# Optimization experiments

Hardware: AMD Instinct MI355X
Metric: run time of the kernel (lower is better)

Reference implementation:

```python
import jax, jax.numpy as jnp
import numpy as np

NEG_SLOPE = 0.2

def gat_conv(x, src, dst, W, a_src, a_dst, b, heads, out_ch, num_nodes):
    # Linear projection per head: [N, H, C]
    h = (x @ W).reshape(num_nodes, heads, out_ch)
    # Per-node attention logits: [N, H]
    s_src = jnp.sum(h * a_src[None, :, :], axis=-1)
    s_dst = jnp.sum(h * a_dst[None, :, :], axis=-1)
    # Per-edge attention score, LeakyReLU(0.2): [E, H]
    e = jax.nn.leaky_relu(s_src[src] + s_dst[dst], negative_slope=NEG_SLOPE)
    # Segment softmax over incoming edges of each destination node
    e_max = jax.ops.segment_max(e, dst, num_segments=num_nodes)
    e_exp = jnp.exp(e - e_max[dst])
    denom = jax.ops.segment_sum(e_exp, dst, num_segments=num_nodes)
    alpha = e_exp / (denom[dst] + 1e-16)  # [E, H]
    # Weighted message aggregation: [N, H, C]
    msg = h[src] * alpha[:, :, None]
    out = jax.ops.segment_sum(msg, dst, num_segments=num_nodes)
    # Concat heads + bias
    return out.reshape(num_nodes, heads * out_ch) + b


def setup_inputs() -> dict:
    key = jax.random.key(0)
    ks = jax.random.split(key, 9)
    N, E = 50000, 1000000
    x = jax.random.normal(ks[0], (N, 300), dtype=jnp.float32)
    edge_index = jax.random.randint(ks[1], (2, E), 0, N, dtype=jnp.int64)
    W1 = jax.random.normal(ks[2], (300, 64), dtype=jnp.float32) * 0.05
    a_src1 = jax.random.normal(ks[3], (8, 8), dtype=jnp.float32) * 0.1
    a_dst1 = jax.random.normal(ks[4], (8, 8), dtype=jnp.float32) * 0.1
    b1 = jnp.zeros((64,), dtype=jnp.float32)
    W2 = jax.random.normal(ks[5], (64, 64), dtype=jnp.float32) * 0.1
    a_src2 = jax.random.normal(ks[6], (1, 64), dtype=jnp.float32) * 0.1
    a_dst2 = jax.random.normal(ks[7], (1, 64), dtype=jnp.float32) * 0.1
    b2 = jnp.zeros((64,), dtype=jnp.float32)
    return {"x": x, "edge_index": edge_index, "W1": W1, "a_src1": a_src1,
            "a_dst1": a_dst1, "b1": b1, "W2": W2, "a_src2": a_src2,
            "a_dst2": a_dst2, "b2": b2}


def reference(x, edge_index, W1, a_src1, a_dst1, b1, W2, a_src2, a_dst2, b2):
    N = x.shape[0]
    src, dst = edge_index[0], edge_index[1]
    # eval mode: dropouts are identity
    h = gat_conv(x, src, dst, W1, a_src1, a_dst1, b1, heads=8, out_ch=8, num_nodes=N)
    h = jax.nn.elu(h)
    out = gat_conv(h, src, dst, W2, a_src2, a_dst2, b2, heads=1, out_ch=64, num_nodes=N)
    return out
```

## Files before the change

### kernel.cpp

```cpp
#include <hip/hip_runtime.h>
#include <math.h>

#define NN 50000
#define NE 1000000
#define NCB 977
#define NGB 782
#define TOTB (NCB + NGB)

typedef __bf16 bf16x8 __attribute__((ext_vector_type(8)));
typedef float f32x4 __attribute__((ext_vector_type(4)));

__device__ inline unsigned short f2bf(float f) {
    unsigned u = __float_as_uint(f);
    u += 0x7FFFu + ((u >> 16) & 1u);
    return (unsigned short)(u >> 16);
}
__device__ inline float bf2f(unsigned short s) {
    return __uint_as_float(((unsigned)s) << 16);
}
__device__ inline float bflo(unsigned r) { return __uint_as_float(r << 16); }
__device__ inline float bfhi(unsigned r) { return __uint_as_float(r & 0xffff0000u); }

__global__ __launch_bounds__(256) void prep_init(const float* __restrict__ W1,
        const float* __restrict__ W2, unsigned short* __restrict__ Bt1,
        unsigned short* __restrict__ Bt2, int* __restrict__ cnt)
{
    int bid = blockIdx.x;
    if (bid < 96) {
        int t = bid * 256 + threadIdx.x;
        if (t < 64 * 320) {
            int c = t / 320, k = t % 320;
            Bt1[t] = (k < 300) ? f2bf(W1[k * 64 + c]) : (unsigned short)0;
        } else {
            int i = t - 64 * 320;
            int c = i >> 6, k = i & 63;
            Bt2[i] = f2bf(W2[k * 64 + c]);
        }
    } else {
        int idx = (bid - 96) * 256 + threadIdx.x;
        int4 z = {0, 0, 0, 0};
        for (int i = idx; i < NN * 4; i += 64 * 256)
            ((int4*)cnt)[i] = z;
    }
}

__global__ __launch_bounds__(256) void k1_count_gemm(
        const int* __restrict__ ei, int* __restrict__ cnt,
        unsigned char* __restrict__ pos,
        const float* __restrict__ A, const unsigned short* __restrict__ Bt,
        unsigned short* __restrict__ hb,
        const float* __restrict__ asrc, const float* __restrict__ adst,
        float* __restrict__ ss, float* __restrict__ sd)
{
    __shared__ unsigned short lds[5120];
    const int tid = threadIdx.x;
    const int bid = blockIdx.x;
    int cidx, gidx;
    if (bid < 2 * NGB) {
        if (bid & 1) { gidx = bid >> 1; cidx = -1; }
        else         { cidx = bid >> 1; gidx = -1; }
    } else { cidx = NGB + (bid - 2 * NGB); gidx = -1; }

    if (cidx >= 0) {
        int e = (cidx * 256 + tid) * 4;
        if (e >= NE) return;
        int4 d = *(const int4*)(ei + NE + e);
        int p0 = atomicAdd(&cnt[d.x << 4], 1);
        int p1 = atomicAdd(&cnt[d.y << 4], 1);
        int p2 = atomicAdd(&cnt[d.z << 4], 1);
        int p3 = atomicAdd(&cnt[d.w << 4], 1);
        uchar4 pk;
        pk.x = (unsigned char)p0; pk.y = (unsigned char)p1;
        pk.z = (unsigned char)p2; pk.w = (unsigned char)p3;
        *(uchar4*)(pos + e) = pk;
        return;
    }

    const int row0 = gidx * 64;
    const int lane = tid & 63, w = tid >> 6;
    const int quad = lane >> 4, mm = lane & 15;
    const int sr = tid >> 2, q8 = (tid & 3) * 8;
    const int gsr = row0 + sr;
    const int K = 300, KT = 10, Kpad = 320, M = NN;

    f32x4 acc[4];
    #pragma unroll
    for (int i = 0; i < 4; ++i) acc[i] = (f32x4){0.f, 0.f, 0.f, 0.f};

    for (int kt = 0; kt < KT; ++kt) {
        const int k0 = kt * 32;
        int4 apack = {0, 0, 0, 0};
        if (gsr < M) {
            const float* ap = A + (size_t)gsr * K + k0 + q8;
            unsigned short* up = (unsigned short*)&apack;
            if (k0 + q8 + 7 < K) {
                float4 v0 = *(const float4*)ap;
                float4 v1 = *(const float4*)(ap + 4);
                up[0]=f2bf(v0.x); up[1]=f2bf(v0.y); up[2]=f2bf(v0.z); up[3]=f2bf(v0.w);
                up[4]=f2bf(v1.x); up[5]=f2bf(v1.y); up[6]=f2bf(v1.z); up[7]=f2bf(v1.w);
            } else {
                #pragma unroll
                for (int j = 0; j < 8; ++j)
                    up[j] = (k0 + q8 + j < K) ? f2bf(ap[j]) : (unsigned short)0;
            }
        }
        *(int4*)(lds + sr * 40 + q8) = apack;
        *(int4*)(lds + 2560 + sr * 40 + q8) =
            *(const int4*)(Bt + (size_t)sr * Kpad + k0 + q8);
        __syncthreads();
        bf16x8 af = *(const bf16x8*)(lds + (w * 16 + mm) * 40 + quad * 8);
        #pragma unroll
        for (int nt = 0; nt < 4; ++nt) {
            bf16x8 bfv = *(const bf16x8*)(lds + 2560 + (nt * 16 + mm) * 40 + quad * 8);
            acc[nt] = __builtin_amdgcn_mfma_f32_16x16x32_bf16(af, bfv, acc[nt], 0, 0, 0);
        }
        __syncthreads();
    }
    #pragma unroll
    for (int nt = 0; nt < 4; ++nt)
        #pragma unroll
        for (int reg = 0; reg < 4; ++reg)
            lds[w * 1152 + (quad * 4 + reg) * 72 + nt * 16 + mm] = f2bf(acc[nt][reg]);
    __syncthreads();
    const int cg = (tid & 3) * 16;
    const unsigned short* crow = lds + (sr >> 4) * 1152 + (sr & 15) * 72;
    if (gsr < M) {
        *(int4*)(hb + (size_t)gsr * 64 + cg)     = *(const int4*)(crow + cg);
        *(int4*)(hb + (size_t)gsr * 64 + cg + 8) = *(const int4*)(crow + cg + 8);
    }
    #pragma unroll
    for (int hh = 0; hh < 2; ++hh) {
        int hd = (tid & 3) + hh * 4;
        float pss = 0.f, psd = 0.f;
        #pragma unroll
        for (int c = 0; c < 8; ++c) {
            float hv = bf2f(crow[hd * 8 + c]);
            pss += hv * asrc[hd * 8 + c];
            psd += hv * adst[hd * 8 + c];
        }
        if (gsr < M) { ss[gsr * 8 + hd] = pss; sd[gsr * 8 + hd] = psd; }
    }
}

__global__ __launch_bounds__(256) void gemm_l2(const unsigned short* __restrict__ A,
        const unsigned short* __restrict__ Bt, unsigned short* __restrict__ hb,
        const float* __restrict__ asrc, const float* __restrict__ adst,
        float* __restrict__ ss, float* __restrict__ sd)
{
    __shared__ unsigned short lds[5120];
    const int tid  = threadIdx.x;
    const int row0 = blockIdx.x * 64;
    const int lane = tid & 63, w = tid >> 6;
    const int quad = lane >> 4, mm = lane & 15;
    const int sr = tid >> 2, q8 = (tid & 3) * 8;
    const int gsr = row0 + sr;
    const int K = 64, KT = 2, Kpad = 64, M = NN;

    f32x4 acc[4];
    #pragma unroll
    for (int i = 0; i < 4; ++i) acc[i] = (f32x4){0.f, 0.f, 0.f, 0.f};

    for (int kt = 0; kt < KT; ++kt) {
        const int k0 = kt * 32;
        int4 apack = {0, 0, 0, 0};
        if (gsr < M) apack = *(const int4*)(A + (size_t)gsr * K + k0 + q8);
        *(int4*)(lds + sr * 40 + q8) = apack;
        *(int4*)(lds + 2560 + sr * 40 + q8) =
            *(const int4*)(Bt + (size_t)sr * Kpad + k0 + q8);
        __syncthreads();
        bf16x8 af = *(const bf16x8*)(lds + (w * 16 + mm) * 40 + quad * 8);
        #pragma unroll
        for (int nt = 0; nt < 4; ++nt) {
            bf16x8 bfv = *(const bf16x8*)(lds + 2560 + (nt * 16 + mm) * 40 + quad * 8);
            acc[nt] = __builtin_amdgcn_mfma_f32_16x16x32_bf16(af, bfv, acc[nt], 0, 0, 0);
        }
        __syncthreads();
    }
    #pragma unroll
    for (int nt = 0; nt < 4; ++nt)
        #pragma unroll
        for (int reg = 0; reg < 4; ++reg)
            lds[w * 1152 + (quad * 4 + reg) * 72 + nt * 16 + mm] = f2bf(acc[nt][reg]);
    __syncthreads();
    const int cg = (tid & 3) * 16;
    const unsigned short* crow = lds + (sr >> 4) * 1152 + (sr & 15) * 72;
    if (gsr < M) {
        *(int4*)(hb + (size_t)gsr * 64 + cg)     = *(const int4*)(crow + cg);
        *(int4*)(hb + (size_t)gsr * 64 + cg + 8) = *(const int4*)(crow + cg + 8);
    }
    int p = tid & 3;
    float pss = 0.f, psd = 0.f;
    #pragma unroll
    for (int c = 0; c < 16; ++c) {
        float hv = bf2f(crow[p * 16 + c]);
        pss += hv * asrc[p * 16 + c];
        psd += hv * adst[p * 16 + c];
    }
    pss += __shfl_xor(pss, 1); psd += __shfl_xor(psd, 1);
    pss += __shfl_xor(pss, 2); psd += __shfl_xor(psd, 2);
    if (p == 0 && gsr < M) { ss[gsr] = pss; sd[gsr] = psd; }
}

__global__ __launch_bounds__(1024) void scan1(const int* __restrict__ cnt,
        int* __restrict__ excl, int* __restrict__ sums)
{
    __shared__ int buf[1024];
    int tid = threadIdx.x;
    int i = blockIdx.x * 1024 + tid;
    int v = (i < NN) ? cnt[i << 4] : 0;
    buf[tid] = v;
    __syncthreads();
    #pragma unroll
    for (int off = 1; off < 1024; off <<= 1) {
        int t = (tid >= off) ? buf[tid - off] : 0;
        __syncthreads();
        buf[tid] += t;
        __syncthreads();
    }
    if (i < NN) excl[i] = buf[tid] - v;
    if (tid == 1023) sums[blockIdx.x] = buf[1023];
}

__global__ __launch_bounds__(1024) void scan23(const int* __restrict__ excl,
        const int* __restrict__ sums, int* __restrict__ rowptr)
{
    int off = 0;
    for (int j = 0; j < (int)blockIdx.x; ++j) off += sums[j];
    int i = blockIdx.x * 1024 + threadIdx.x;
    if (i < NN) rowptr[i] = excl[i] + off;
    if (i == 0) rowptr[NN] = NE;
}

__global__ __launch_bounds__(256) void scatter_k(const int* __restrict__ ei,
        const int* __restrict__ rowptr, const unsigned char* __restrict__ pos,
        unsigned short* __restrict__ col)
{
    int e = (blockIdx.x * 256 + threadIdx.x) * 4;
    if (e >= NE) return;
    int4 s = *(const int4*)(ei + e);
    int4 d = *(const int4*)(ei + NE + e);
    uchar4 p = *(const uchar4*)(pos + e);
    int r0 = rowptr[d.x], r1 = rowptr[d.y], r2 = rowptr[d.z], r3 = rowptr[d.w];
    col[r0 + p.x] = (unsigned short)s.x;
    col[r1 + p.y] = (unsigned short)s.y;
    col[r2 + p.z] = (unsigned short)s.z;
    col[r3 + p.w] = (unsigned short)s.w;
}

#define LEAKY(s) ((s) > 0.f ? (s) : 0.2f * (s))

__global__ __launch_bounds__(256) void agg_l1(const int* __restrict__ rowptr,
        const unsigned short* __restrict__ col, const unsigned short* __restrict__ hb,
        const float* __restrict__ ss, const float* __restrict__ sd,
        const float* __restrict__ b, unsigned short* __restrict__ out)
{
    int n = (blockIdx.x * 256 + threadIdx.x) >> 6;
    int lane = threadIdx.x & 63;
    if (n >= NN) return;
    const int es = lane >> 4;
    const int cg = (lane & 15) << 2;
    const int hd = cg >> 3;
    float sdst = sd[n * 8 + hd];
    int r0 = rowptr[n], r1 = rowptr[n + 1];
    f32x4 acc = {0.f, 0.f, 0.f, 0.f};
    float dsum = 0.f;
    for (int i = r0; i < r1; i += 16) {
        int av[4]; bool vv[4];
        #pragma unroll
        for (int u = 0; u < 4; ++u) {
            int e = i + u * 4 + es;
            vv[u] = e < r1;
            av[u] = (int)col[vv[u] ? e : r0];
        }
        uint2 rr[4]; float sv[4];
        #pragma unroll
        for (int u = 0; u < 4; ++u) {
            rr[u] = *(const uint2*)(hb + av[u] * 64 + cg);
            sv[u] = ss[av[u] * 8 + hd];
        }
        #pragma unroll
        for (int u = 0; u < 4; ++u) {
            float wv = vv[u] ? __expf(LEAKY(sv[u] + sdst)) : 0.f;
            acc[0] += wv * bflo(rr[u].x);
            acc[1] += wv * bfhi(rr[u].x);
            acc[2] += wv * bflo(rr[u].y);
            acc[3] += wv * bfhi(rr[u].y);
            dsum += wv;
        }
    }
    #pragma unroll
    for (int m = 16; m <= 32; m <<= 1) {
        acc[0] += __shfl_xor(acc[0], m); acc[1] += __shfl_xor(acc[1], m);
        acc[2] += __shfl_xor(acc[2], m); acc[3] += __shfl_xor(acc[3], m);
        dsum += __shfl_xor(dsum, m);
    }
    if (es == 0) {
        float inv = 1.f / (dsum + 1e-16f);
        float v0 = acc[0] * inv + b[cg + 0]; v0 = v0 > 0.f ? v0 : __expf(v0) - 1.f;
        float v1 = acc[1] * inv + b[cg + 1]; v1 = v1 > 0.f ? v1 : __expf(v1) - 1.f;
        float v2 = acc[2] * inv + b[cg + 2]; v2 = v2 > 0.f ? v2 : __expf(v2) - 1.f;
        float v3 = acc[3] * inv + b[cg + 3]; v3 = v3 > 0.f ? v3 : __expf(v3) - 1.f;
        unsigned o01 = (unsigned)f2bf(v0) | ((unsigned)f2bf(v1) << 16);
        unsigned o23 = (unsigned)f2bf(v2) | ((unsigned)f2bf(v3) << 16);
        *(uint2*)(out + n * 64 + cg) = make_uint2(o01, o23);
    }
}

__global__ __launch_bounds__(256) void agg_l2(const int* __restrict__ rowptr,
        const unsigned short* __restrict__ col, const unsigned short* __restrict__ hb,
        const float* __restrict__ ss, const float* __restrict__ sd,
        const float* __restrict__ b, float* __restrict__ out)
{
    int n = (blockIdx.x * 256 + threadIdx.x) >> 6;
    int lane = threadIdx.x & 63;
    if (n >= NN) return;
    const int es = lane >> 4;
    const int cg = (lane & 15) << 2;
    float sdst = sd[n];
    int r0 = rowptr[n], r1 = rowptr[n + 1];
    f32x4 acc = {0.f, 0.f, 0.f, 0.f};
    float dsum = 0.f;
    for (int i = r0; i < r1; i += 16) {
        int av[4]; bool vv[4];
        #pragma unroll
        for (int u = 0; u < 4; ++u) {
            int e = i + u * 4 + es;
            vv[u] = e < r1;
            av[u] = (int)col[vv[u] ? e : r0];
        }
        uint2 rr[4]; float sv[4];
        #pragma unroll
        for (int u = 0; u < 4; ++u) {
            rr[u] = *(const uint2*)(hb + av[u] * 64 + cg);
            sv[u] = ss[av[u]];
        }
        #pragma unroll
        for (int u = 0; u < 4; ++u) {
            float wv = vv[u] ? __expf(LEAKY(sv[u] + sdst)) : 0.f;
            acc[0] += wv * bflo(rr[u].x);
            acc[1] += wv * bfhi(rr[u].x);
            acc[2] += wv * bflo(rr[u].y);
            acc[3] += wv * bfhi(rr[u].y);
            dsum += wv;
        }
    }
    #pragma unroll
    for (int m = 16; m <= 32; m <<= 1) {
        acc[0] += __shfl_xor(acc[0], m); acc[1] += __shfl_xor(acc[1], m);
        acc[2] += __shfl_xor(acc[2], m); acc[3] += __shfl_xor(acc[3], m);
        dsum += __shfl_xor(dsum, m);
    }
    if (es == 0) {
        float inv = 1.f / (dsum + 1e-16f);
        float4 o;
        o.x = acc[0] * inv + b[cg + 0];
        o.y = acc[1] * inv + b[cg + 1];
        o.z = acc[2] * inv + b[cg + 2];
        o.w = acc[3] * inv + b[cg + 3];
        *(float4*)(out + n * 64 + cg) = o;
    }
}

extern "C" void kernel_launch(void* const* d_in, const int* in_sizes, int n_in,
                              void* d_out, int out_size, void* d_ws, size_t ws_size,
                              hipStream_t stream)
{
    const float* x      = (const float*)d_in[0];
    const int*   ei     = (const int*)d_in[1];
    const float* W1     = (const float*)d_in[2];
    const float* a_src1 = (const float*)d_in[3];
    const float* a_dst1 = (const float*)d_in[4];
    const float* b1     = (const float*)d_in[5];
    const float* W2     = (const float*)d_in[6];
    const float* a_src2 = (const float*)d_in[7];
    const float* a_dst2 = (const float*)d_in[8];
    const float* b2     = (const float*)d_in[9];
    float* out = (float*)d_out;

    char* wp = (char*)d_ws;
    unsigned short* hb  = (unsigned short*)wp;  wp += (size_t)NN * 64 * 2;
    unsigned short* P1b = (unsigned short*)wp;  wp += (size_t)NN * 64 * 2;
    unsigned short* Bt1 = (unsigned short*)wp;  wp += (size_t)64 * 320 * 2;
    unsigned short* Bt2 = (unsigned short*)wp;  wp += (size_t)64 * 64 * 2;
    float* ss1 = (float*)wp;  wp += (size_t)NN * 8 * 4;
    float* sd1 = (float*)wp;  wp += (size_t)NN * 8 * 4;
    int* cnt    = (int*)wp;  wp += (size_t)NN * 64;
    int* excl   = (int*)wp;  wp += (size_t)NN * 4;
    int* sums   = (int*)wp;  wp += 64 * 4;
    int* rowptr = (int*)wp;  wp += (size_t)(NN + 4) * 4;
    unsigned short* col = (unsigned short*)wp;  wp += (size_t)(NE + 8) * 2;
    unsigned char*  pos = (unsigned char*)wp;   wp += (size_t)NE;
    float* ss2 = ss1;
    float* sd2 = ss1 + NN;

    const int NB = (NN + 1023) / 1024;

    prep_init<<<160, 256, 0, stream>>>(W1, W2, Bt1, Bt2, cnt);
    k1_count_gemm<<<TOTB, 256, 0, stream>>>(
        ei, cnt, pos, x, Bt1, hb, a_src1, a_dst1, ss1, sd1);
    scan1<<<NB, 1024, 0, stream>>>(cnt, excl, sums);
    scan23<<<NB, 1024, 0, stream>>>(excl, sums, rowptr);
    scatter_k<<<(NE / 4 + 255) / 256, 256, 0, stream>>>(ei, rowptr, pos, col);

    agg_l1<<<(NN * 64 + 255) / 256, 256, 0, stream>>>(rowptr, col, hb, ss1, sd1, b1, P1b);
    gemm_l2<<<(NN + 63) / 64, 256, 0, stream>>>(P1b, Bt2, hb, a_src2, a_dst2, ss2, sd2);
    agg_l2<<<(NN * 64 + 255) / 256, 256, 0, stream>>>(rowptr, col, hb, ss2, sd2, b2, out);
}
```

Baseline: 246.3 us.

## Replace global atomic degree counting with LDS-privatized per-chunk histograms

Edge destination counting now runs in 128 blocks, each owning one edge chunk and one node range, and counts with shared-memory atomics instead of global atomics on padded counters. Per-chunk counts go to global memory, and scan1 builds per-node prefix offsets across chunks, which scatter adds when placing CSR columns. This removes global atomic contention and the counter-zeroing pass. In exchange, every counting block reads its whole edge chunk while keeping only 1/8 of it, and a 3.2MB prefix array is added that scatter must gather from.

```diff
diff --git a/kernel.cpp b/kernel.cpp
--- a/kernel.cpp
+++ b/kernel.cpp
@@ -3,9 +3,14 @@
 
 #define NN 50000
 #define NE 1000000
-#define NCB 977
+#define EC 16
+#define CSH 16
+#define WR 8
+#define RNG 6250
+#define RPAD 6272
+#define NCNT (EC * WR)
 #define NGB 782
-#define TOTB (NCB + NGB)
+#define TOTB (NCNT + NGB)
 
 typedef __bf16 bf16x8 __attribute__((ext_vector_type(8)));
 typedef float f32x4 __attribute__((ext_vector_type(4)));
@@ -23,24 +28,16 @@
 
 __global__ __launch_bounds__(256) void prep_init(const float* __restrict__ W1,
         const float* __restrict__ W2, unsigned short* __restrict__ Bt1,
-        unsigned short* __restrict__ Bt2, int* __restrict__ cnt)
-{
-    int bid = blockIdx.x;
-    if (bid < 96) {
-        int t = bid * 256 + threadIdx.x;
-        if (t < 64 * 320) {
-            int c = t / 320, k = t % 320;
-            Bt1[t] = (k < 300) ? f2bf(W1[k * 64 + c]) : (unsigned short)0;
-        } else {
-            int i = t - 64 * 320;
-            int c = i >> 6, k = i & 63;
-            Bt2[i] = f2bf(W2[k * 64 + c]);
-        }
+        unsigned short* __restrict__ Bt2)
+{
+    int t = blockIdx.x * 256 + threadIdx.x;
+    if (t < 64 * 320) {
+        int c = t / 320, k = t % 320;
+        Bt1[t] = (k < 300) ? f2bf(W1[k * 64 + c]) : (unsigned short)0;
     } else {
-        int idx = (bid - 96) * 256 + threadIdx.x;
-        int4 z = {0, 0, 0, 0};
-        for (int i = idx; i < NN * 4; i += 64 * 256)
-            ((int4*)cnt)[i] = z;
+        int i = t - 64 * 320;
+        int c = i >> 6, k = i & 63;
+        Bt2[i] = f2bf(W2[k * 64 + c]);
     }
 }
 
@@ -52,31 +49,36 @@
         const float* __restrict__ asrc, const float* __restrict__ adst,
         float* __restrict__ ss, float* __restrict__ sd)
 {
-    __shared__ unsigned short lds[5120];
+    __shared__ __align__(16) int sm[RNG];
     const int tid = threadIdx.x;
     const int bid = blockIdx.x;
-    int cidx, gidx;
-    if (bid < 2 * NGB) {
-        if (bid & 1) { gidx = bid >> 1; cidx = -1; }
-        else         { cidx = bid >> 1; gidx = -1; }
-    } else { cidx = NGB + (bid - 2 * NGB); gidx = -1; }
-
-    if (cidx >= 0) {
-        int e = (cidx * 256 + tid) * 4;
-        if (e >= NE) return;
-        int4 d = *(const int4*)(ei + NE + e);
-        int p0 = atomicAdd(&cnt[d.x << 4], 1);
-        int p1 = atomicAdd(&cnt[d.y << 4], 1);
-        int p2 = atomicAdd(&cnt[d.z << 4], 1);
-        int p3 = atomicAdd(&cnt[d.w << 4], 1);
-        uchar4 pk;
-        pk.x = (unsigned char)p0; pk.y = (unsigned char)p1;
-        pk.z = (unsigned char)p2; pk.w = (unsigned char)p3;
-        *(uchar4*)(pos + e) = pk;
+
+    if (bid < NCNT) {
+        const int c = bid >> 3, w = bid & 7;
+        const int lo = w * RNG;
+        for (int j = tid; j < RNG; j += 256) sm[j] = 0;
+        __syncthreads();
+        const int base = c << CSH;
+        for (int it = 0; it < (1 << CSH) / 1024; ++it) {
+            int e = base + (it * 256 + tid) * 4;
+            if (e < NE) {
+                int4 d = *(const int4*)(ei + NE + e);
+                unsigned t0 = (unsigned)(d.x - lo), t1 = (unsigned)(d.y - lo);
+                unsigned t2 = (unsigned)(d.z - lo), t3 = (unsigned)(d.w - lo);
+                if (t0 < RNG) pos[e]     = (unsigned char)atomicAdd(&sm[t0], 1);
+                if (t1 < RNG) pos[e + 1] = (unsigned char)atomicAdd(&sm[t1], 1);
+                if (t2 < RNG) pos[e + 2] = (unsigned char)atomicAdd(&sm[t2], 1);
+                if (t3 < RNG) pos[e + 3] = (unsigned char)atomicAdd(&sm[t3], 1);
+            }
+        }
+        __syncthreads();
+        int* dstp = cnt + (size_t)bid * RPAD;
+        for (int j = tid; j < RNG; j += 256) dstp[j] = sm[j];
         return;
     }
 
-    const int row0 = gidx * 64;
+    unsigned short* lds = (unsigned short*)sm;
+    const int row0 = (bid - NCNT) * 64;
     const int lane = tid & 63, w = tid >> 6;
     const int quad = lane >> 4, mm = lane & 15;
     const int sr = tid >> 2, q8 = (tid & 3) * 8;
@@ -202,12 +204,28 @@
 }
 
 __global__ __launch_bounds__(1024) void scan1(const int* __restrict__ cnt,
-        int* __restrict__ excl, int* __restrict__ sums)
+        int* __restrict__ excl, int* __restrict__ sums, int* __restrict__ rpre)
 {
     __shared__ int buf[1024];
     int tid = threadIdx.x;
     int i = blockIdx.x * 1024 + tid;
-    int v = (i < NN) ? cnt[i << 4] : 0;
+    int v = 0;
+    if (i < NN) {
+        int w = i / RNG;
+        int j = i - w * RNG;
+        int run = 0;
+        int pre[EC];
+        #pragma unroll
+        for (int c = 0; c < EC; ++c) {
+            pre[c] = run;
+            run += cnt[(size_t)(c * 8 + w) * RPAD + j];
+        }
+        v = run;
+        #pragma unroll
+        for (int q = 0; q < EC / 4; ++q)
+            *(int4*)(rpre + (size_t)i * EC + q * 4) =
+                make_int4(pre[q * 4], pre[q * 4 + 1], pre[q * 4 + 2], pre[q * 4 + 3]);
+    }
     buf[tid] = v;
     __syncthreads();
     #pragma unroll
@@ -233,18 +251,22 @@
 
 __global__ __launch_bounds__(256) void scatter_k(const int* __restrict__ ei,
         const int* __restrict__ rowptr, const unsigned char* __restrict__ pos,
-        unsigned short* __restrict__ col)
+        const int* __restrict__ rpre, unsigned short* __restrict__ col)
 {
     int e = (blockIdx.x * 256 + threadIdx.x) * 4;
     if (e >= NE) return;
+    int c = e >> CSH;
     int4 s = *(const int4*)(ei + e);
     int4 d = *(const int4*)(ei + NE + e);
     uchar4 p = *(const uchar4*)(pos + e);
-    int r0 = rowptr[d.x], r1 = rowptr[d.y], r2 = rowptr[d.z], r3 = rowptr[d.w];
-    col[r0 + p.x] = (unsigned short)s.x;
-    col[r1 + p.y] = (unsigned short)s.y;
-    col[r2 + p.z] = (unsigned short)s.z;
-    col[r3 + p.w] = (unsigned short)s.w;
+    int r0 = rowptr[d.x] + rpre[(d.x << 4) + c] + p.x;
+    int r1 = rowptr[d.y] + rpre[(d.y << 4) + c] + p.y;
+    int r2 = rowptr[d.z] + rpre[(d.z << 4) + c] + p.z;
+    int r3 = rowptr[d.w] + rpre[(d.w << 4) + c] + p.w;
+    col[r0] = (unsigned short)s.x;
+    col[r1] = (unsigned short)s.y;
+    col[r2] = (unsigned short)s.z;
+    col[r3] = (unsigned short)s.w;
 }
 
 #define LEAKY(s) ((s) > 0.f ? (s) : 0.2f * (s))
@@ -384,7 +406,8 @@
     unsigned short* Bt2 = (unsigned short*)wp;  wp += (size_t)64 * 64 * 2;
     float* ss1 = (float*)wp;  wp += (size_t)NN * 8 * 4;
     float* sd1 = (float*)wp;  wp += (size_t)NN * 8 * 4;
-    int* cnt    = (int*)wp;  wp += (size_t)NN * 64;
+    int* cnt    = (int*)wp;  wp += (size_t)NCNT * RPAD * 4;
+    int* rpre   = (int*)wp;  wp += (size_t)NN * EC * 4;
     int* excl   = (int*)wp;  wp += (size_t)NN * 4;
     int* sums   = (int*)wp;  wp += 64 * 4;
     int* rowptr = (int*)wp;  wp += (size_t)(NN + 4) * 4;
@@ -395,12 +418,12 @@
 
     const int NB = (NN + 1023) / 1024;
 
-    prep_init<<<160, 256, 0, stream>>>(W1, W2, Bt1, Bt2, cnt);
+    prep_init<<<96, 256, 0, stream>>>(W1, W2, Bt1, Bt2);
     k1_count_gemm<<<TOTB, 256, 0, stream>>>(
         ei, cnt, pos, x, Bt1, hb, a_src1, a_dst1, ss1, sd1);
-    scan1<<<NB, 1024, 0, stream>>>(cnt, excl, sums);
+    scan1<<<NB, 1024, 0, stream>>>(cnt, excl, sums, rpre);
     scan23<<<NB, 1024, 0, stream>>>(excl, sums, rowptr);
-    scatter_k<<<(NE / 4 + 255) / 256, 256, 0, stream>>>(ei, rowptr, pos, col);
+    scatter_k<<<(NE / 4 + 255) / 256, 256, 0, stream>>>(ei, rowptr, pos, rpre, col);
 
     agg_l1<<<(NN * 64 + 255) / 256, 256, 0, stream>>>(rowptr, col, hb, ss1, sd1, b1, P1b);
     gemm_l2<<<(NN + 63) / 64, 256, 0, stream>>>(P1b, Bt2, hb, a_src2, a_dst2, ss2, sd2);
```

Result: slower. 254.1 us (+3.2%).
